# Optimization experiments

Hardware: AMD Instinct MI355X
Metric: run time of the kernel (lower is better)

## Reference

```python
import jax, jax.numpy as jnp
import numpy as np

B, S, D, H, E = 2, 2048, 1024, 16, 8
DH = D // H
CAP_FACTOR = 1.2


def setup_inputs() -> dict:
    key = jax.random.key(0)
    ks = jax.random.split(key, 14)
    s = 0.02
    return {
        "embed": jax.random.normal(ks[0], (B, S, D), jnp.float32),
        "Wq": jax.random.normal(ks[1], (H, DH, D), jnp.float32) * s,
        "bq": jnp.zeros((H, DH), jnp.float32),
        "Wk": jax.random.normal(ks[2], (H, DH, D), jnp.float32) * s,
        "bk": jnp.zeros((H, DH), jnp.float32),
        "Wv": jax.random.normal(ks[3], (H, DH, D), jnp.float32) * s,
        "bv": jnp.zeros((H, DH), jnp.float32),
        "We": jax.random.normal(ks[4], (E, D, D), jnp.float32) * s,
        "be": jnp.zeros((E, D), jnp.float32),
        "Wsw": jax.random.normal(ks[5], (E, D), jnp.float32) * s,
        "bsw": jnp.zeros((E,), jnp.float32),
        "gamma": jnp.ones((D,), jnp.float32),
        "beta": jnp.zeros((D,), jnp.float32),
    }


def _forward(embed, Wq, bq, Wk, bk, Wv, bv, We, be, Wsw, bsw, gamma, beta):
    b, s, d = embed.shape
    h, e = Wq.shape[0], We.shape[0]
    # --- multi-head attention (all heads batched via einsum) ---
    q = jnp.einsum('bsd,hed->bhse', embed, Wq) + bq[None, :, None, :]
    k = jnp.einsum('bsd,hed->bhse', embed, Wk) + bk[None, :, None, :]
    v = jnp.einsum('bsd,hed->bhse', embed, Wv) + bv[None, :, None, :]
    att = jnp.einsum('bhse,bhte->bhst', q, k)  # [b,h,s,s]
    tril = jnp.tril(jnp.ones((s, s), bool))
    # faithful: upper triangle zeroed (NOT -inf), scale by sqrt(embedding_dim)
    att = jnp.where(tril, att, 0.0) / jnp.sqrt(jnp.float32(d))
    att = jax.nn.softmax(att, axis=-1)
    out = jnp.einsum('bhst,bhte->bhse', att, v)
    hiddens = out.transpose(0, 2, 1, 3).reshape(b, s, d)
    # --- SwitchLinear: top-1 token-choice routing with capacity drop ---
    x = hiddens.reshape(-1, d)  # [N, d]
    n = b * s
    capacity = int(CAP_FACTOR * n / e)
    logits = x @ Wsw.T + bsw
    probs = jax.nn.softmax(logits, axis=-1)
    route_probs = jnp.max(probs, axis=-1)
    routes = jnp.argmax(probs, axis=-1)
    onehot = jax.nn.one_hot(routes, e, dtype=jnp.int32)
    pos = jnp.cumsum(onehot, axis=0) - 1  # position within chosen expert
    pos = jnp.take_along_axis(pos, routes[:, None], axis=1)[:, 0]
    kept = pos < capacity
    slot = jnp.where(kept, routes * capacity + pos, e * capacity)  # overflow row
    dispatch = jnp.zeros((e * capacity + 1, d), x.dtype).at[slot].set(x)
    expert_in = dispatch[: e * capacity].reshape(e, capacity, d)
    expert_out = jnp.einsum('ecd,efd->ecf', expert_in, We) + be[:, None, :]
    expert_flat = jnp.concatenate(
        [expert_out.reshape(e * capacity, d), jnp.zeros((1, d), x.dtype)], 0)
    gathered = expert_flat[slot]
    y = jnp.where(kept[:, None], gathered, x)  # dropped tokens pass through
    y = (y * route_probs[:, None]).reshape(b, s, d)
    # --- residual + LayerNorm ---
    x2 = y + embed
    mean = jnp.mean(x2, axis=-1, keepdims=True)
    var = jnp.var(x2, axis=-1, keepdims=True)
    return (x2 - mean) / jnp.sqrt(var + 1e-5) * gamma + beta


def reference(embed, Wq, bq, Wk, bk, Wv, bv, We, be, Wsw, bsw, gamma, beta):
    return _forward(embed, Wq, bq, Wk, bk, Wv, bv, We, be, Wsw, bsw, gamma, beta)
```

## Files before the change

kernel.cpp:

```cpp
#include <hip/hip_runtime.h>

constexpr int B = 2, S = 2048, D = 1024, H = 16, E = 8, DH = 64;
constexpr int N = B * S;
constexpr int CAP = 614;
constexpr int ECAP = 640;
constexpr float INV_SQRT_D = 0.03125f;

typedef __bf16 bf16x8 __attribute__((ext_vector_type(8)));
typedef float f32x4 __attribute__((ext_vector_type(4)));
typedef unsigned int u32x4 __attribute__((ext_vector_type(4)));

__device__ __forceinline__ ushort f2bf(float x) {
  __bf16 h = (__bf16)x;
  return __builtin_bit_cast(unsigned short, h);
}
__device__ __forceinline__ float bf2f(ushort u) {
  __bf16 h = __builtin_bit_cast(__bf16, u);
  return (float)h;
}
__device__ __forceinline__ void gld16(const void* g, void* l) {
  __builtin_amdgcn_global_load_lds(
      (const __attribute__((address_space(1))) unsigned int*)g,
      (__attribute__((address_space(3))) unsigned int*)l, 16, 0, 0);
}

__global__ __launch_bounds__(256) void cvt_pair(const float* __restrict__ in,
                                                ushort* __restrict__ out)
{
  const long long idx4 = (long long)blockIdx.x * 256 + threadIdx.x;
  const float4 xv = ((const float4*)in)[idx4];
  const long long row = idx4 >> 8;
  const int col = (int)((idx4 & 255) << 2);
  float xs[4] = {xv.x, xv.y, xv.z, xv.w};
  ushort4 hi, lo;
  ushort* hp = (ushort*)&hi; ushort* lp = (ushort*)&lo;
  #pragma unroll
  for (int c = 0; c < 4; ++c) {
    ushort h = f2bf(xs[c]);
    hp[c] = h;
    lp[c] = f2bf(xs[c] - bf2f(h));
  }
  *(ushort4*)&out[row * 2048 + col] = hi;
  *(ushort4*)&out[row * 2048 + 1024 + col] = lo;
}

__global__ __launch_bounds__(256) void cvt_plain(const float* __restrict__ in,
                                                 ushort* __restrict__ out)
{
  const long long idx4 = (long long)blockIdx.x * 256 + threadIdx.x;
  const float4 xv = ((const float4*)in)[idx4];
  ushort4 o;
  o.x = f2bf(xv.x); o.y = f2bf(xv.y); o.z = f2bf(xv.z); o.w = f2bf(xv.w);
  *(ushort4*)&out[idx4 * 4] = o;
}

__global__ __launch_bounds__(256) void qkv_gemm(
    const ushort* __restrict__ A, const ushort* __restrict__ Wp,
    const float* __restrict__ bq, const float* __restrict__ bk,
    const float* __restrict__ bv, ushort* __restrict__ pairout)
{
  __shared__ char smem[32768] __attribute__((aligned(128)));
  const int tid = threadIdx.x;
  const int lane = tid & 63;
  const int lrow = lane & 15;
  const int lk = lane >> 4;
  const int wv = tid >> 6;
  const int rAc = (wv >> 1) * 64;
  const int rBc = (wv & 1) * 64;
  const int flat = (int)(blockIdx.y * 24 + blockIdx.x);
  const int swz = (flat & 7) * 96 + (flat >> 3);
  const int bn0 = (swz % 24) * 128;
  const int bm0 = (swz / 24) * 128;
  const int z = bn0 >> 10;
  const ushort* Wt = Wp + (long long)z * (1024 * 2048) +
                     (long long)(bn0 & 1023) * 2048;
  const float* bp = (z == 0) ? bq : (z == 1) ? bk : bv;
  const int srow = tid >> 3;
  const int su = tid & 7;

  f32x4 acc[4][4] = {};

  for (int step = 0; step < 48; ++step) {
    const int k0 = step * 64;
    const int srcA = (k0 < 2048) ? k0 : k0 - 2048;
    const int srcB = (k0 < 1024) ? k0 : k0 - 1024;
    __syncthreads();
    #pragma unroll
    for (int i = 0; i < 4; ++i) {
      const int row = i * 32 + srow;
      const int u = su ^ (row & 7);
      gld16(A + (long long)(bm0 + row) * 2048 + srcA + u * 8,
            smem + i * 4096 + wv * 1024);
      gld16(Wt + (long long)row * 2048 + srcB + u * 8,
            smem + 16384 + i * 4096 + wv * 1024);
    }
    asm volatile("s_waitcnt vmcnt(0)" ::: "memory");
    __syncthreads();
    #pragma unroll
    for (int h = 0; h < 2; ++h) {
      bf16x8 af[4], bfr[4];
      #pragma unroll
      for (int i = 0; i < 4; ++i) {
        const int row = rAc + i * 16 + lrow;
        const int u = (h * 4 + lk) ^ (row & 7);
        af[i] = *(const bf16x8*)(smem + row * 128 + u * 16);
      }
      #pragma unroll
      for (int j = 0; j < 4; ++j) {
        const int row = rBc + j * 16 + lrow;
        const int u = (h * 4 + lk) ^ (row & 7);
        bfr[j] = *(const bf16x8*)(smem + 16384 + row * 128 + u * 16);
      }
      #pragma unroll
      for (int i = 0; i < 4; ++i)
        #pragma unroll
        for (int j = 0; j < 4; ++j)
          acc[i][j] = __builtin_amdgcn_mfma_f32_16x16x32_bf16(
              af[i], bfr[j], acc[i][j], 0, 0, 0);
    }
  }
  const int rg = lk * 4;
  #pragma unroll
  for (int j = 0; j < 4; ++j) {
    const int col = bn0 + rBc + j * 16 + lrow;
    const int cz = col & 1023;
    const float bj = bp[cz];
    const int hh = cz >> 6, e = cz & 63;
    #pragma unroll
    for (int i = 0; i < 4; ++i) {
      const int rbase = bm0 + rAc + i * 16 + rg;
      const int b = rbase >> 11;
      if (z < 2) {
        const int sbase = rbase & 2047;
        ushort* dst = pairout + (long long)z * 8388608 +
                      ((long long)(b * 16 + hh) * 2048 + sbase) * 128 + e;
        #pragma unroll
        for (int r = 0; r < 4; ++r) {
          float val = acc[i][j][r] + bj;
          ushort vh = f2bf(val);
          dst[r * 128] = vh;
          dst[r * 128 + 64] = f2bf(val - bf2f(vh));
        }
      } else {
        const int tb = rbase & 2047;
        ushort4 hi4, lo4;
        ushort* hp = (ushort*)&hi4; ushort* lp = (ushort*)&lo4;
        #pragma unroll
        for (int r = 0; r < 4; ++r) {
          float val = acc[i][j][r] + bj;
          ushort vh = f2bf(val);
          hp[r] = vh;
          lp[r] = f2bf(val - bf2f(vh));
        }
        ushort* vdst = pairout + 2ll * 8388608 +
                       (long long)(b * 16 + hh) * 262144 +
                       (long long)e * 2048 + tb;
        *(ushort4*)vdst = hi4;
        *(ushort4*)(vdst + 131072) = lo4;
      }
    }
  }
}

__global__ __launch_bounds__(256) void expert_gemm(
    const ushort* __restrict__ A, const ushort* __restrict__ W,
    const float* __restrict__ be, float* __restrict__ C)
{
  __shared__ char smem[32768] __attribute__((aligned(128)));
  const int z = blockIdx.z;
  A += (long long)z * (ECAP * D);
  W += (long long)z * (D * D);
  C += (long long)z * (ECAP * D);
  const float* bp = be + (long long)z * D;
  const int tid = threadIdx.x;
  const int lane = tid & 63;
  const int lrow = lane & 15;
  const int lk = lane >> 4;
  const int wv = tid >> 6;
  const int rAc = (wv >> 1) * 64;
  const int rBc = (wv & 1) * 64;
  const int bm0 = blockIdx.y * 128;
  const int bn0 = blockIdx.x * 128;
  const int srow = tid >> 3;
  const int su = tid & 7;

  f32x4 acc[4][4] = {};
  for (int step = 0; step < 16; ++step) {
    const int k0 = step * 64;
    __syncthreads();
    #pragma unroll
    for (int i = 0; i < 4; ++i) {
      const int row = i * 32 + srow;
      const int u = su ^ (row & 7);
      gld16(A + (long long)(bm0 + row) * 1024 + k0 + u * 8,
            smem + i * 4096 + wv * 1024);
      gld16(W + (long long)(bn0 + row) * 1024 + k0 + u * 8,
            smem + 16384 + i * 4096 + wv * 1024);
    }
    asm volatile("s_waitcnt vmcnt(0)" ::: "memory");
    __syncthreads();
    #pragma unroll
    for (int h = 0; h < 2; ++h) {
      bf16x8 af[4], bfr[4];
      #pragma unroll
      for (int i = 0; i < 4; ++i) {
        const int row = rAc + i * 16 + lrow;
        const int u = (h * 4 + lk) ^ (row & 7);
        af[i] = *(const bf16x8*)(smem + row * 128 + u * 16);
      }
      #pragma unroll
      for (int j = 0; j < 4; ++j) {
        const int row = rBc + j * 16 + lrow;
        const int u = (h * 4 + lk) ^ (row & 7);
        bfr[j] = *(const bf16x8*)(smem + 16384 + row * 128 + u * 16);
      }
      #pragma unroll
      for (int i = 0; i < 4; ++i)
        #pragma unroll
        for (int j = 0; j < 4; ++j)
          acc[i][j] = __builtin_amdgcn_mfma_f32_16x16x32_bf16(
              af[i], bfr[j], acc[i][j], 0, 0, 0);
    }
  }
  const int rg = lk * 4;
  #pragma unroll
  for (int j = 0; j < 4; ++j) {
    const int col = bn0 + rBc + j * 16 + lrow;
    const float bj = bp[col];
    #pragma unroll
    for (int i = 0; i < 4; ++i) {
      const int rbase = bm0 + rAc + i * 16 + rg;
      #pragma unroll
      for (int r = 0; r < 4; ++r)
        C[(long long)(rbase + r) * 1024 + col] = acc[i][j][r] + bj;
    }
  }
}

__global__ __launch_bounds__(256) void suffix_kernel(const ushort* __restrict__ vtp,
                                                     float* __restrict__ vsuf)
{
  const int R = blockIdx.x;
  const int bh = R >> 6, e = R & 63;
  const ushort* hi = vtp + (long long)bh * 262144 + (long long)e * 2048;
  const ushort* lo = hi + 131072;
  const int tid = threadIdx.x;
  ushort4 h0 = *(const ushort4*)(hi + tid * 8);
  ushort4 h1 = *(const ushort4*)(hi + tid * 8 + 4);
  ushort4 l0 = *(const ushort4*)(lo + tid * 8);
  ushort4 l1 = *(const ushort4*)(lo + tid * 8 + 4);
  float v[8];
  v[0] = bf2f(h0.x) + bf2f(l0.x); v[1] = bf2f(h0.y) + bf2f(l0.y);
  v[2] = bf2f(h0.z) + bf2f(l0.z); v[3] = bf2f(h0.w) + bf2f(l0.w);
  v[4] = bf2f(h1.x) + bf2f(l1.x); v[5] = bf2f(h1.y) + bf2f(l1.y);
  v[6] = bf2f(h1.z) + bf2f(l1.z); v[7] = bf2f(h1.w) + bf2f(l1.w);
  float s = 0.f;
  #pragma unroll
  for (int x = 0; x < 8; ++x) s += v[x];
  __shared__ float ss[256];
  ss[tid] = s;
  __syncthreads();
  for (int off = 1; off < 256; off <<= 1) {
    float t = (tid + off < 256) ? ss[tid + off] : 0.f;
    __syncthreads();
    ss[tid] += t;
    __syncthreads();
  }
  float acc = (tid < 255) ? ss[tid + 1] : 0.f;
  float out[8];
  for (int x = 7; x >= 0; --x) { acc += v[x]; out[x] = acc; }
  #pragma unroll
  for (int x = 0; x < 8; ++x)
    vsuf[(long long)R * 2048 + tid * 8 + x] = out[x];
}

__device__ __forceinline__ void attn_stage_kv(
    const ushort* kbase, const ushort* vbase, int t0,
    char* kdst, char* vdst, int tid, int wv)
{
  #pragma unroll
  for (int i = 0; i < 2; ++i) {
    const int L = i * 512 + tid;
    const int row = L >> 4, u = L & 15;
    gld16(kbase + (long long)(t0 + row) * 128 + ((u ^ (row & 15)) * 8),
          kdst + i * 8192 + wv * 1024);
  }
  #pragma unroll
  for (int i = 0; i < 2; ++i) {
    const int L = i * 512 + tid;
    const int sec = L >> 9, vr = (L >> 3) & 63, u = L & 7;
    gld16(vbase + (long long)sec * 131072 + (long long)vr * 2048 + t0 +
              ((u ^ (vr & 7)) * 8),
          vdst + i * 8192 + wv * 1024);
  }
}

__global__ __launch_bounds__(512, 4) void attn_mfma(
    const ushort* __restrict__ qp, const ushort* __restrict__ kp,
    const ushort* __restrict__ vtp, const float* __restrict__ vsuf,
    float* __restrict__ hid)
{
  __shared__ char smem[65536] __attribute__((aligned(128)));
  const int tid = threadIdx.x;
  const int lane = tid & 63;
  const int wv = tid >> 6;
  const int g = lane >> 4, c = lane & 15;

  const int flat = (int)(blockIdx.y * 16 + blockIdx.x);
  const int swz = (flat & 7) * 64 + (flat >> 3);
  const int bh = swz >> 4;
  const int bx = swz & 15;
  const int qi = ((bh >> 1) & 1) ? (15 - bx) : bx;
  const int sB0 = qi * 128;

  const ushort* qbase = qp + (long long)bh * (2048 * 128);
  const ushort* kbase = kp + (long long)bh * (2048 * 128);
  const ushort* vbase = vtp + (long long)bh * 262144;

  #pragma unroll
  for (int i = 0; i < 4; ++i) {
    const int L = i * 512 + tid;
    const int row = L >> 4, u = L & 15;
    gld16(qbase + (long long)(sB0 + row) * 128 + ((u ^ (row & 15)) * 8),
          smem + i * 8192 + wv * 1024);
  }
  asm volatile("s_waitcnt vmcnt(0)" ::: "memory");
  __builtin_amdgcn_s_barrier();
  bf16x8 qh[2], ql[2];
  {
    const int qrow = wv * 16 + c;
    const ushort* qsl = (const ushort*)smem + qrow * 128;
    #pragma unroll
    for (int h = 0; h < 2; ++h) {
      qh[h] = *(const bf16x8*)(qsl + (((h * 4 + g) ^ c) * 8));
      ql[h] = *(const bf16x8*)(qsl + (((8 + h * 4 + g) ^ c) * 8));
    }
  }
  asm volatile("s_waitcnt lgkmcnt(0)" ::: "memory");
  __builtin_amdgcn_s_barrier();

  attn_stage_kv(kbase, vbase, 0, smem, smem + 32768, tid, wv);

  f32x4 oacc[4] = {};
  float l_acc = 0.f;
  const int nt = 2 * qi + 2;
  const int srcA = ((lane >> 4) & 1) * 32 + c;
  const int srcB = srcA + 16;
  const bool ghi = lane >= 32;

  for (int t = 0; t < nt; ++t) {
    const int t0 = t * 64;
    char* kcur = smem + (t & 1) * 16384;
    char* vcur = smem + 32768 + (t & 1) * 16384;
    if (t + 1 < nt) {
      attn_stage_kv(kbase, vbase, t0 + 64,
                    smem + ((t + 1) & 1) * 16384,
                    smem + 32768 + ((t + 1) & 1) * 16384, tid, wv);
      asm volatile("s_waitcnt vmcnt(4)" ::: "memory");
    } else {
      asm volatile("s_waitcnt vmcnt(0)" ::: "memory");
    }
    __builtin_amdgcn_s_barrier();

    const ushort* ks = (const ushort*)kcur;
    const ushort* vt = (const ushort*)vcur;

    f32x4 acc[4] = {};
    __builtin_amdgcn_s_setprio(1);
    #pragma unroll
    for (int h = 0; h < 2; ++h) {
      #pragma unroll
      for (int j = 0; j < 4; ++j) {
        const int krow = j * 16 + c;
        const ushort* kr = ks + krow * 128;
        bf16x8 kh = *(const bf16x8*)(kr + (((h * 4 + g) ^ c) * 8));
        bf16x8 kl = *(const bf16x8*)(kr + (((8 + h * 4 + g) ^ c) * 8));
        acc[j] = __builtin_amdgcn_mfma_f32_16x16x32_bf16(kh, qh[h], acc[j], 0, 0, 0);
        acc[j] = __builtin_amdgcn_mfma_f32_16x16x32_bf16(kl, qh[h], acc[j], 0, 0, 0);
        acc[j] = __builtin_amdgcn_mfma_f32_16x16x32_bf16(kh, ql[h], acc[j], 0, 0, 0);
      }
    }
    __builtin_amdgcn_s_setprio(0);

    unsigned int pw[16];
    float prt = 0.f;
    const int sg_c = sB0 + wv * 16 + c;
    #pragma unroll
    for (int j = 0; j < 4; ++j)
      #pragma unroll
      for (int r = 0; r < 4; ++r) {
        const int tg = t0 + j * 16 + 4 * g + r;
        float w = (tg <= sg_c) ? __expf(acc[j][r] * INV_SQRT_D) : 0.f;
        prt += w;
        ushort hi = f2bf(w);
        ushort lo = f2bf(w - bf2f(hi));
        pw[j * 4 + r] = (unsigned)hi | ((unsigned)lo << 16);
      }
    prt += __shfl_xor(prt, 16);
    prt += __shfl_xor(prt, 32);
    l_acc += prt;

    unsigned int paw[2][8];
    #pragma unroll
    for (int h = 0; h < 2; ++h)
      #pragma unroll
      for (int r = 0; r < 4; ++r) {
        unsigned a0 = (unsigned)__shfl((int)pw[(2 * h) * 4 + r], srcA);
        unsigned a1 = (unsigned)__shfl((int)pw[(2 * h + 1) * 4 + r], srcA);
        unsigned b0 = (unsigned)__shfl((int)pw[(2 * h) * 4 + r], srcB);
        unsigned b1 = (unsigned)__shfl((int)pw[(2 * h + 1) * 4 + r], srcB);
        paw[h][r] = ghi ? a1 : a0;
        paw[h][4 + r] = ghi ? b1 : b0;
      }
    bf16x8 pah[2], pal[2];
    #pragma unroll
    for (int h = 0; h < 2; ++h) {
      u32x4 hv, lv;
      #pragma unroll
      for (int p = 0; p < 4; ++p) {
        hv[p] = (paw[h][2 * p] & 0xffffu) | (paw[h][2 * p + 1] << 16);
        lv[p] = (paw[h][2 * p] >> 16) | (paw[h][2 * p + 1] & 0xffff0000u);
      }
      pah[h] = __builtin_bit_cast(bf16x8, hv);
      pal[h] = __builtin_bit_cast(bf16x8, lv);
    }

    __builtin_amdgcn_s_setprio(1);
    #pragma unroll
    for (int h = 0; h < 2; ++h)
      #pragma unroll
      for (int j = 0; j < 4; ++j) {
        const int vrow = j * 16 + c;
        const ushort* vr = vt + vrow * 64;
        bf16x8 vh = *(const bf16x8*)(vr + (((h * 4 + g) ^ (c & 7)) * 8));
        bf16x8 vl = *(const bf16x8*)(vr + 4096 + (((h * 4 + g) ^ (c & 7)) * 8));
        oacc[j] = __builtin_amdgcn_mfma_f32_16x16x32_bf16(pah[h], vh, oacc[j], 0, 0, 0);
        oacc[j] = __builtin_amdgcn_mfma_f32_16x16x32_bf16(pal[h], vh, oacc[j], 0, 0, 0);
        oacc[j] = __builtin_amdgcn_mfma_f32_16x16x32_bf16(pah[h], vl, oacc[j], 0, 0, 0);
      }
    __builtin_amdgcn_s_setprio(0);
    asm volatile("s_waitcnt lgkmcnt(0)" ::: "memory");
    __builtin_amdgcn_s_barrier();
  }

  const int b = bh >> 4, hh = bh & 15;
  #pragma unroll
  for (int r = 0; r < 4; ++r) {
    const float lr = __shfl(l_acc, (lane & 48) | (4 * g + r));
    const int sg = sB0 + wv * 16 + 4 * g + r;
    const float denom = lr + (float)(S - 1 - sg);
    #pragma unroll
    for (int j = 0; j < 4; ++j) {
      const int e = j * 16 + c;
      const float suf = (sg + 1 < S) ? vsuf[((long long)bh * 64 + e) * 2048 + sg + 1] : 0.f;
      hid[(long long)(b * S + sg) * 1024 + hh * 64 + e] = (oacc[j][r] + suf) / denom;
    }
  }
}

__global__ __launch_bounds__(256) void router_kernel(
    const float* __restrict__ x, const float* __restrict__ Wsw,
    const float* __restrict__ bsw, int* __restrict__ routes,
    float* __restrict__ rprob)
{
  const int w = threadIdx.x >> 6, lane = threadIdx.x & 63;
  const int i = blockIdx.x * 4 + w;
  float p[E] = {};
  const float4* xr = (const float4*)(x + (long long)i * D);
  #pragma unroll
  for (int t = 0; t < 4; ++t) {
    float4 xv = xr[lane + 64 * t];
    #pragma unroll
    for (int e = 0; e < E; ++e) {
      float4 wv = ((const float4*)(Wsw + e * D))[lane + 64 * t];
      p[e] += xv.x * wv.x + xv.y * wv.y + xv.z * wv.z + xv.w * wv.w;
    }
  }
  #pragma unroll
  for (int off = 32; off; off >>= 1)
    #pragma unroll
    for (int e = 0; e < E; ++e) p[e] += __shfl_xor(p[e], off);
  if (lane == 0) {
    float m = -1e30f; int arg = 0;
    #pragma unroll
    for (int e = 0; e < E; ++e) {
      float l = p[e] + bsw[e];
      if (l > m) { m = l; arg = e; }
      p[e] = l;
    }
    float sum = 0.f;
    #pragma unroll
    for (int e = 0; e < E; ++e) sum += __expf(p[e] - m);
    routes[i] = arg;
    rprob[i] = 1.f / sum;
  }
}

__global__ __launch_bounds__(256) void scan_kernel(const int* __restrict__ routes,
                                                   int* __restrict__ slot)
{
  __shared__ int hist[256][E];
  const int tid = threadIdx.x;
  const int per = N / 256;
  int cnt[E] = {};
  for (int j = 0; j < per; ++j) cnt[routes[tid * per + j]]++;
  #pragma unroll
  for (int e = 0; e < E; ++e) hist[tid][e] = cnt[e];
  __syncthreads();
  if (tid < E) {
    int run = 0;
    for (int t = 0; t < 256; ++t) { int tmp = hist[t][tid]; hist[t][tid] = run; run += tmp; }
  }
  __syncthreads();
  int run[E];
  #pragma unroll
  for (int e = 0; e < E; ++e) run[e] = hist[tid][e];
  for (int j = 0; j < per; ++j) {
    int i = tid * per + j;
    int r = routes[i];
    int pos = run[r]++;
    slot[i] = (pos < CAP) ? r * ECAP + pos : -1;
  }
}

__global__ __launch_bounds__(256) void dispatch_kernel(
    const float* __restrict__ x, const int* __restrict__ slot,
    ushort* __restrict__ expert_in)
{
  const int i = blockIdx.x;
  const int sl = slot[i];
  if (sl < 0) return;
  float4 xv = ((const float4*)&x[(long long)i * D])[threadIdx.x];
  ushort4 o;
  o.x = f2bf(xv.x); o.y = f2bf(xv.y); o.z = f2bf(xv.z); o.w = f2bf(xv.w);
  ((ushort4*)&expert_in[(long long)sl * D])[threadIdx.x] = o;
}

__global__ __launch_bounds__(256) void finalize_kernel(
    const float* __restrict__ x, const float* __restrict__ eout,
    const int* __restrict__ slot, const float* __restrict__ rprob,
    const float* __restrict__ embed, const float* __restrict__ gamma,
    const float* __restrict__ beta, float* __restrict__ out)
{
  const int i = blockIdx.x;
  const int tid = threadIdx.x;
  const int sl = slot[i];
  const float rp = rprob[i];
  const float4* src = (sl >= 0) ? (const float4*)&eout[(long long)sl * D]
                                : (const float4*)&x[(long long)i * D];
  float4 yv = src[tid];
  float4 ev = ((const float4*)&embed[(long long)i * D])[tid];
  float v0 = yv.x * rp + ev.x;
  float v1 = yv.y * rp + ev.y;
  float v2 = yv.z * rp + ev.z;
  float v3 = yv.w * rp + ev.w;
  float s1 = v0 + v1 + v2 + v3;
  float s2 = v0*v0 + v1*v1 + v2*v2 + v3*v3;
  #pragma unroll
  for (int off = 32; off; off >>= 1) {
    s1 += __shfl_xor(s1, off);
    s2 += __shfl_xor(s2, off);
  }
  __shared__ float wsum[4], wsq[4];
  const int wid = tid >> 6, lid = tid & 63;
  if (lid == 0) { wsum[wid] = s1; wsq[wid] = s2; }
  __syncthreads();
  float tot  = wsum[0] + wsum[1] + wsum[2] + wsum[3];
  float tot2 = wsq[0] + wsq[1] + wsq[2] + wsq[3];
  const float mean = tot * (1.f / D);
  const float var = tot2 * (1.f / D) - mean * mean;
  const float rstd = rsqrtf(var + 1e-5f);
  float4 gv = ((const float4*)gamma)[tid];
  float4 bv = ((const float4*)beta)[tid];
  float4 ov;
  ov.x = (v0 - mean) * rstd * gv.x + bv.x;
  ov.y = (v1 - mean) * rstd * gv.y + bv.y;
  ov.z = (v2 - mean) * rstd * gv.z + bv.z;
  ov.w = (v3 - mean) * rstd * gv.w + bv.w;
  ((float4*)&out[(long long)i * D])[tid] = ov;
}

extern "C" void kernel_launch(void* const* d_in, const int* in_sizes, int n_in,
                              void* d_out, int out_size, void* d_ws, size_t ws_size,
                              hipStream_t stream) {
  const float* embed = (const float*)d_in[0];
  const float* Wq = (const float*)d_in[1];
  const float* bq = (const float*)d_in[2];
  const float* Wk = (const float*)d_in[3];
  const float* bk = (const float*)d_in[4];
  const float* Wv = (const float*)d_in[5];
  const float* bv = (const float*)d_in[6];
  const float* We = (const float*)d_in[7];
  const float* be = (const float*)d_in[8];
  const float* Wsw = (const float*)d_in[9];
  const float* bsw = (const float*)d_in[10];
  const float* gamma = (const float*)d_in[11];
  const float* beta = (const float*)d_in[12];
  float* out = (float*)d_out;

  char* base = (char*)d_ws;
  ushort* epair      = (ushort*)base;
  float*  hid        = (float*)base;
  ushort* wpair      = (ushort*)(base + 16777216);
  ushort* expert_in  = (ushort*)(base + 16777216);
  ushort* pairs      = (ushort*)(base + 29360128);
  float*  expert_out = (float*)(base + 29360128);
  ushort* qp  = pairs;
  ushort* kp  = pairs + 8388608;
  ushort* vtp = pairs + 2 * 8388608;
  float*  vsuf = (float*)(base + 79691776);
  ushort* webf = (ushort*)(base + 79691776);
  int*    routes = (int*)(base + 96468992);
  int*    slot   = routes + N;
  float*  rprob  = (float*)(slot + N);

  cvt_pair<<<N * D / 1024, 256, 0, stream>>>(embed, epair);
  cvt_pair<<<D * D / 1024, 256, 0, stream>>>(Wq, wpair + 0ll * D * 2048);
  cvt_pair<<<D * D / 1024, 256, 0, stream>>>(Wk, wpair + 1ll * D * 2048);
  cvt_pair<<<D * D / 1024, 256, 0, stream>>>(Wv, wpair + 2ll * D * 2048);
  qkv_gemm<<<dim3(24, 32), 256, 0, stream>>>(epair, wpair, bq, bk, bv, pairs);
  suffix_kernel<<<B * H * 64, 256, 0, stream>>>(vtp, vsuf);
  attn_mfma<<<dim3(16, 32), 512, 0, stream>>>(qp, kp, vtp, vsuf, hid);
  router_kernel<<<N / 4, 256, 0, stream>>>(hid, Wsw, bsw, routes, rprob);
  scan_kernel<<<1, 256, 0, stream>>>(routes, slot);
  cvt_plain<<<(int)((long long)E * D * D / 1024), 256, 0, stream>>>(We, webf);
  dispatch_kernel<<<N, 256, 0, stream>>>(hid, slot, expert_in);
  expert_gemm<<<dim3(8, ECAP / 128, E), 256, 0, stream>>>(
      expert_in, webf, be, expert_out);
  finalize_kernel<<<N, 256, 0, stream>>>(hid, expert_out, slot, rprob,
                                         embed, gamma, beta, out);
}
```

Baseline: 404.7 us.

## Replace per-position V suffix sums with chunk suffix sums and fuse conversions

The masked upper-triangle entries (score zero, exp weight one) inside the diagonal block are now folded into the MFMA P·V product by setting their weight to 1. That leaves only a per-128-chunk suffix sum of V, replacing the full per-position suffix scan and its large vsuf array. The four fp32-to-bf16 pair conversion launches are merged into one kernel, and the qkv_gemm tile-to-XCD mapping is changed so each XCD owns three adjacent N tiles. This cuts suffix-scan work, memory traffic and launch overhead, at the cost of a small extra two-kernel chunk reduction.

```diff
diff --git a/kernel.cpp b/kernel.cpp
--- a/kernel.cpp
+++ b/kernel.cpp
@@ -24,13 +24,27 @@
       (__attribute__((address_space(3))) unsigned int*)l, 16, 0, 0);
 }
 
-__global__ __launch_bounds__(256) void cvt_pair(const float* __restrict__ in,
-                                                ushort* __restrict__ out)
+__global__ __launch_bounds__(256) void cvt_all(
+    const float* __restrict__ embed, const float* __restrict__ Wq,
+    const float* __restrict__ Wk, const float* __restrict__ Wv,
+    ushort* __restrict__ epair, ushort* __restrict__ wpair)
 {
   const long long idx4 = (long long)blockIdx.x * 256 + threadIdx.x;
-  const float4 xv = ((const float4*)in)[idx4];
-  const long long row = idx4 >> 8;
+  const int row = (int)(idx4 >> 8);
   const int col = (int)((idx4 & 255) << 2);
+  const float* src;
+  ushort* dst;
+  if (row < 4096) {
+    src = embed + (long long)row * 1024;
+    dst = epair + (long long)row * 2048;
+  } else {
+    const int r2 = row - 4096;
+    const int z = r2 >> 10;
+    const float* w = (z == 0) ? Wq : (z == 1) ? Wk : Wv;
+    src = w + (long long)(r2 & 1023) * 1024;
+    dst = wpair + (long long)r2 * 2048;
+  }
+  const float4 xv = *(const float4*)(src + col);
   float xs[4] = {xv.x, xv.y, xv.z, xv.w};
   ushort4 hi, lo;
   ushort* hp = (ushort*)&hi; ushort* lp = (ushort*)&lo;
@@ -40,8 +54,8 @@
     hp[c] = h;
     lp[c] = f2bf(xs[c] - bf2f(h));
   }
-  *(ushort4*)&out[row * 2048 + col] = hi;
-  *(ushort4*)&out[row * 2048 + 1024 + col] = lo;
+  *(ushort4*)&dst[col] = hi;
+  *(ushort4*)&dst[1024 + col] = lo;
 }
 
 __global__ __launch_bounds__(256) void cvt_plain(const float* __restrict__ in,
@@ -68,9 +82,10 @@
   const int rAc = (wv >> 1) * 64;
   const int rBc = (wv & 1) * 64;
   const int flat = (int)(blockIdx.y * 24 + blockIdx.x);
-  const int swz = (flat & 7) * 96 + (flat >> 3);
-  const int bn0 = (swz % 24) * 128;
-  const int bm0 = (swz / 24) * 128;
+  const int xcd = flat & 7;
+  const int sub = flat >> 3;
+  const int bn0 = (xcd * 3 + sub % 3) * 128;
+  const int bm0 = (sub / 3) * 128;
   const int z = bn0 >> 10;
   const ushort* Wt = Wp + (long long)z * (1024 * 2048) +
                      (long long)(bn0 & 1023) * 2048;
@@ -237,41 +252,35 @@
   }
 }
 
-__global__ __launch_bounds__(256) void suffix_kernel(const ushort* __restrict__ vtp,
-                                                     float* __restrict__ vsuf)
-{
-  const int R = blockIdx.x;
-  const int bh = R >> 6, e = R & 63;
-  const ushort* hi = vtp + (long long)bh * 262144 + (long long)e * 2048;
-  const ushort* lo = hi + 131072;
-  const int tid = threadIdx.x;
-  ushort4 h0 = *(const ushort4*)(hi + tid * 8);
-  ushort4 h1 = *(const ushort4*)(hi + tid * 8 + 4);
-  ushort4 l0 = *(const ushort4*)(lo + tid * 8);
-  ushort4 l1 = *(const ushort4*)(lo + tid * 8 + 4);
-  float v[8];
-  v[0] = bf2f(h0.x) + bf2f(l0.x); v[1] = bf2f(h0.y) + bf2f(l0.y);
-  v[2] = bf2f(h0.z) + bf2f(l0.z); v[3] = bf2f(h0.w) + bf2f(l0.w);
-  v[4] = bf2f(h1.x) + bf2f(l1.x); v[5] = bf2f(h1.y) + bf2f(l1.y);
-  v[6] = bf2f(h1.z) + bf2f(l1.z); v[7] = bf2f(h1.w) + bf2f(l1.w);
+__global__ __launch_bounds__(64) void vchunk_sum(const ushort* __restrict__ vtp,
+                                                 float* __restrict__ csum)
+{
+  const int bh = blockIdx.x, c = blockIdx.y, e = threadIdx.x;
+  const ushort* base = vtp + (long long)bh * 262144 + (long long)e * 2048 + c * 128;
   float s = 0.f;
   #pragma unroll
-  for (int x = 0; x < 8; ++x) s += v[x];
-  __shared__ float ss[256];
-  ss[tid] = s;
-  __syncthreads();
-  for (int off = 1; off < 256; off <<= 1) {
-    float t = (tid + off < 256) ? ss[tid + off] : 0.f;
-    __syncthreads();
-    ss[tid] += t;
-    __syncthreads();
-  }
-  float acc = (tid < 255) ? ss[tid + 1] : 0.f;
-  float out[8];
-  for (int x = 7; x >= 0; --x) { acc += v[x]; out[x] = acc; }
-  #pragma unroll
-  for (int x = 0; x < 8; ++x)
-    vsuf[(long long)R * 2048 + tid * 8 + x] = out[x];
+  for (int sec = 0; sec < 2; ++sec) {
+    const ushort* p = base + sec * 131072;
+    for (int i = 0; i < 16; ++i) {
+      ushort4 a = *(const ushort4*)(p + i * 8);
+      ushort4 b = *(const ushort4*)(p + i * 8 + 4);
+      s += bf2f(a.x) + bf2f(a.y) + bf2f(a.z) + bf2f(a.w);
+      s += bf2f(b.x) + bf2f(b.y) + bf2f(b.z) + bf2f(b.w);
+    }
+  }
+  csum[((long long)bh * 16 + c) * 64 + e] = s;
+}
+
+__global__ __launch_bounds__(64) void vchunk_suffix(const float* __restrict__ csum,
+                                                    float* __restrict__ vsufC)
+{
+  const int bh = blockIdx.x, e = threadIdx.x;
+  float acc = 0.f;
+  vsufC[((long long)bh * 17 + 16) * 64 + e] = 0.f;
+  for (int c = 15; c >= 0; --c) {
+    acc += csum[((long long)bh * 16 + c) * 64 + e];
+    vsufC[((long long)bh * 17 + c) * 64 + e] = acc;
+  }
 }
 
 __device__ __forceinline__ void attn_stage_kv(
@@ -297,7 +306,7 @@
 
 __global__ __launch_bounds__(512, 4) void attn_mfma(
     const ushort* __restrict__ qp, const ushort* __restrict__ kp,
-    const ushort* __restrict__ vtp, const float* __restrict__ vsuf,
+    const ushort* __restrict__ vtp, const float* __restrict__ vsufC,
     float* __restrict__ hid)
 {
   __shared__ char smem[65536] __attribute__((aligned(128)));
@@ -390,7 +399,7 @@
       #pragma unroll
       for (int r = 0; r < 4; ++r) {
         const int tg = t0 + j * 16 + 4 * g + r;
-        float w = (tg <= sg_c) ? __expf(acc[j][r] * INV_SQRT_D) : 0.f;
+        float w = (tg <= sg_c) ? __expf(acc[j][r] * INV_SQRT_D) : 1.0f;
         prt += w;
         ushort hi = f2bf(w);
         ushort lo = f2bf(w - bf2f(hi));
@@ -444,16 +453,18 @@
   }
 
   const int b = bh >> 4, hh = bh & 15;
+  const float tailcnt = (float)(S - (qi + 1) * 128);
+  const float* sufp = vsufC + ((long long)bh * 17 + (qi + 1)) * 64;
   #pragma unroll
   for (int r = 0; r < 4; ++r) {
     const float lr = __shfl(l_acc, (lane & 48) | (4 * g + r));
     const int sg = sB0 + wv * 16 + 4 * g + r;
-    const float denom = lr + (float)(S - 1 - sg);
+    const float denom = lr + tailcnt;
     #pragma unroll
     for (int j = 0; j < 4; ++j) {
       const int e = j * 16 + c;
-      const float suf = (sg + 1 < S) ? vsuf[((long long)bh * 64 + e) * 2048 + sg + 1] : 0.f;
-      hid[(long long)(b * S + sg) * 1024 + hh * 64 + e] = (oacc[j][r] + suf) / denom;
+      hid[(long long)(b * S + sg) * 1024 + hh * 64 + e] =
+          (oacc[j][r] + sufp[e]) / denom;
     }
   }
 }
@@ -608,19 +619,18 @@
   ushort* qp  = pairs;
   ushort* kp  = pairs + 8388608;
   ushort* vtp = pairs + 2 * 8388608;
-  float*  vsuf = (float*)(base + 79691776);
-  ushort* webf = (ushort*)(base + 79691776);
-  int*    routes = (int*)(base + 96468992);
+  float*  csum   = (float*)(base + 79691776);
+  float*  vsufC  = (float*)(base + 79691776 + 131072);
+  ushort* webf   = (ushort*)(base + 79691776 + 524288);
+  int*    routes = (int*)(base + 97255424);
   int*    slot   = routes + N;
   float*  rprob  = (float*)(slot + N);
 
-  cvt_pair<<<N * D / 1024, 256, 0, stream>>>(embed, epair);
-  cvt_pair<<<D * D / 1024, 256, 0, stream>>>(Wq, wpair + 0ll * D * 2048);
-  cvt_pair<<<D * D / 1024, 256, 0, stream>>>(Wk, wpair + 1ll * D * 2048);
-  cvt_pair<<<D * D / 1024, 256, 0, stream>>>(Wv, wpair + 2ll * D * 2048);
+  cvt_all<<<7168, 256, 0, stream>>>(embed, Wq, Wk, Wv, epair, wpair);
   qkv_gemm<<<dim3(24, 32), 256, 0, stream>>>(epair, wpair, bq, bk, bv, pairs);
-  suffix_kernel<<<B * H * 64, 256, 0, stream>>>(vtp, vsuf);
-  attn_mfma<<<dim3(16, 32), 512, 0, stream>>>(qp, kp, vtp, vsuf, hid);
+  vchunk_sum<<<dim3(32, 16), 64, 0, stream>>>(vtp, csum);
+  vchunk_suffix<<<32, 64, 0, stream>>>(csum, vsufC);
+  attn_mfma<<<dim3(16, 32), 512, 0, stream>>>(qp, kp, vtp, vsufC, hid);
   router_kernel<<<N / 4, 256, 0, stream>>>(hid, Wsw, bsw, routes, rprob);
   scan_kernel<<<1, 256, 0, stream>>>(routes, slot);
   cvt_plain<<<(int)((long long)E * D * D / 1024), 256, 0, stream>>>(We, webf);
```

New measurement: 387.8 us. -4.2%, faster.
